# Performance work log

Measured on AMD Instinct MI355X. Metric: run time of the kernel, lower is better.

The kernel has to match this reference:

```python
import jax, jax.numpy as jnp
import numpy as np

NUM_CLASSES = 21
EPS = 1e-6


def setup_inputs() -> dict:
    key = jax.random.key(0)
    k1, k2, k3 = jax.random.split(key, 3)
    feats = jax.random.normal(k1, (8, 256, 64, 64), dtype=jnp.float32)
    preds = jax.random.normal(k2, (8, NUM_CLASSES, 256, 256), dtype=jnp.float32)
    # labels in [0, 22): includes nclass=21 which acts as an ignore label
    masks = jax.random.randint(k3, (8, 256, 256), 0, 22, dtype=jnp.int64)
    return {"feats": feats, "preds": preds, "masks": masks}


def reference(feats, preds, masks):
    B, C = feats.shape[0], feats.shape[1]
    H, W = masks.shape[-2:]
    K = NUM_CLASSES

    # argmax over class logits -> predicted label map [B, H, W]
    pred_lbl = jnp.argmax(preds, axis=1)

    # bilinear upsample (align_corners=False, matches half-pixel resize)
    feats_up = jax.image.resize(feats, (B, C, H, W), method="bilinear")

    cls = jnp.arange(K)
    # one-hot of gt mask and of predictions; labels >= K (incl. 255) fall in
    # the dropped last channel of one_hot_2d, i.e. match no class here.
    gt_oh = (masks[:, None, :, :] == cls[None, :, None, None])      # [B,K,H,W]
    pr_oh = (pred_lbl[:, None, :, :] == cls[None, :, None, None])   # [B,K,H,W]
    joint = (gt_oh & pr_oh).astype(feats_up.dtype)                  # [B,K,H,W]

    counts = joint.sum(axis=(2, 3))                                  # [B,K]
    sums = jnp.einsum("bchw,bkhw->bkc", feats_up, joint)            # [B,K,C]

    # per-image class means (absent classes -> 0/eps = 0), then batch mean
    proto = (sums / (counts[..., None] + EPS)).mean(axis=0)          # [K,C]
    return proto
```

## Files before the change

kernel.cpp:

```cpp
#include <hip/hip_runtime.h>

#define KC   21
#define BB   8
#define CC   256
#define HWP  65536
#define SRC  4096
#define NS   32
#define PC   128

#define WSF_COUNTS 131072
#define WSF_ACC2   131328
#define ZTOT_F4    ((256 + BB*KC*CC) / 4)

__global__ __launch_bounds__(256, 2)
void k1_classify(const float* __restrict__ preds,
                 const int*   __restrict__ masks,
                 unsigned char* __restrict__ L,
                 float* __restrict__ zbase)
{
    int tid = threadIdx.x;
    int idx = blockIdx.x * 256 + tid;

    if (idx < ZTOT_F4)
        reinterpret_cast<float4*>(zbase)[idx] = make_float4(0.f, 0.f, 0.f, 0.f);

    int b   = idx >> 14;
    int hw4 = (idx & 16383) << 2;

    const float* pb = preds + (size_t)b * KC * HWP + hw4;
    float va[4][KC];
#pragma unroll
    for (int k = 0; k < KC; ++k) {
        float4 t = *reinterpret_cast<const float4*>(pb + (size_t)k * HWP);
        va[0][k] = t.x; va[1][k] = t.y; va[2][k] = t.z; va[3][k] = t.w;
    }

    int4 mm = *reinterpret_cast<const int4*>(masks + b * HWP + hw4);
    int mk[4] = { mm.x, mm.y, mm.z, mm.w };

    uchar4 r;
    unsigned char* rp = reinterpret_cast<unsigned char*>(&r);
#pragma unroll
    for (int j = 0; j < 4; ++j) {
        float best = va[j][0];
        int   bi   = 0;
#pragma unroll
        for (int k = 1; k < KC; ++k) {
            if (va[j][k] > best) { best = va[j][k]; bi = k; }
        }
        rp[j] = (mk[j] == bi) ? (unsigned char)bi : (unsigned char)255;
    }
    *reinterpret_cast<uchar4*>(L + (size_t)b * HWP + hw4) = r;
}

__global__ __launch_bounds__(1024, 4)
void k2_contract(const float* __restrict__ feats,
                 const unsigned char* __restrict__ L,
                 float* __restrict__ acc2,
                 float* __restrict__ counts)
{
    __shared__ float ws[KC * PC];
    __shared__ float scr[3 * KC * CC];
    int s = blockIdx.x, b = blockIdx.y;
    int tid = threadIdx.x;
    int p0 = s * PC;
    int ybase = 2 * s;

    int cp   = tid & 255;
    int psub = tid >> 8;
    int pw   = psub * 32;

    for (int t = tid; t < KC * PC / 4; t += 1024)
        *reinterpret_cast<float4*>(ws + t * 4) = make_float4(0.f, 0.f, 0.f, 0.f);

    float f[32];
    {
        const float* frow = feats + (size_t)(b * CC + cp) * SRC + p0 + pw;
#pragma unroll
        for (int q = 0; q < 8; ++q) {
            float4 t = *reinterpret_cast<const float4*>(frow + q * 4);
            f[q * 4 + 0] = t.x; f[q * 4 + 1] = t.y;
            f[q * 4 + 2] = t.z; f[q * 4 + 3] = t.w;
        }
    }
    __syncthreads();

    {
        int r = tid >> 6, cb = tid & 63;
        int h = 8 * s - 2 + r;
        if (r < 12 && (unsigned)h < 256u) {
            float sy = h * 0.25f - 0.375f;
            int   yt = (int)floorf(sy);
            float wy = sy - (float)yt;
            int ya = yt < 0 ? 0 : yt;
            int yb = yt + 1 > 63 ? 63 : yt + 1;
            float wyy0 = ((ya == ybase)     ? (1.f - wy) : 0.f) + ((yb == ybase)     ? wy : 0.f);
            float wyy1 = ((ya == ybase + 1) ? (1.f - wy) : 0.f) + ((yb == ybase + 1) ? wy : 0.f);
            if (wyy0 != 0.f || wyy1 != 0.f) {
                const unsigned char* Lrow = L + ((size_t)b << 16) + ((size_t)h << 8);
#pragma unroll
                for (int j = 0; j < 4; ++j) {
                    int w = cb + j * 64;
                    int k = Lrow[w];
                    if (k < KC) {
                        float sx = w * 0.25f - 0.375f;
                        int   xt = (int)floorf(sx);
                        float wx = sx - (float)xt;
                        int xa = xt < 0 ? 0 : xt;
                        int xb = xt + 1 > 63 ? 63 : xt + 1;
                        float* wk = ws + k * PC;
                        if (wyy0 != 0.f) {
                            atomicAdd(wk + xa, wyy0 * (1.f - wx));
                            atomicAdd(wk + xb, wyy0 * wx);
                        }
                        if (wyy1 != 0.f) {
                            atomicAdd(wk + 64 + xa, wyy1 * (1.f - wx));
                            atomicAdd(wk + 64 + xb, wyy1 * wx);
                        }
                    }
                }
            }
        }
    }
    __syncthreads();

    if (tid < KC) {
        float swcnt = 0.f;
#pragma unroll
        for (int i = 0; i < PC; ++i)
            swcnt += ws[tid * PC + ((i + tid * 8) & (PC - 1))];
        if (swcnt != 0.f)
            atomicAdd(&counts[b * KC + tid], swcnt);
    }

    float acc[KC];
#pragma unroll
    for (int k = 0; k < KC; ++k) {
        const float* wk = ws + k * PC + pw;
        float a0 = 0.f, a1 = 0.f, a2 = 0.f, a3 = 0.f;
#pragma unroll
        for (int q = 0; q < 8; ++q) {
            float4 w4 = *reinterpret_cast<const float4*>(wk + q * 4);
            a0 += w4.x * f[q * 4 + 0];
            a1 += w4.y * f[q * 4 + 1];
            a2 += w4.z * f[q * 4 + 2];
            a3 += w4.w * f[q * 4 + 3];
        }
        acc[k] = (a0 + a1) + (a2 + a3);
    }

    if (psub >= 1) {
        float* sp = scr + (psub - 1) * (KC * CC);
#pragma unroll
        for (int k = 0; k < KC; ++k) sp[k * CC + cp] = acc[k];
    }
    __syncthreads();
    if (psub == 0) {
        float* ap = acc2 + (size_t)(b * KC) * CC + cp;
#pragma unroll
        for (int k = 0; k < KC; ++k) {
            float v = acc[k] + scr[k * CC + cp]
                             + scr[KC * CC + k * CC + cp]
                             + scr[2 * KC * CC + k * CC + cp];
            atomicAdd(ap + (size_t)k * CC, v);
        }
    }
}

__global__ __launch_bounds__(256)
void k3_finalize(const float* __restrict__ acc2,
                 const float* __restrict__ counts,
                 float* __restrict__ out)
{
    int k = blockIdx.x;
    int c = threadIdx.x;

    float r = 0.f;
#pragma unroll
    for (int b = 0; b < BB; ++b) {
        float cnt = counts[b * KC + k];
        r += acc2[(size_t)(b * KC + k) * CC + c] / (cnt + 1e-6f);
    }
    out[k * CC + c] = r * 0.125f;
}

extern "C" void kernel_launch(void* const* d_in, const int* in_sizes, int n_in,
                              void* d_out, int out_size, void* d_ws, size_t ws_size,
                              hipStream_t stream) {
    const float* feats = (const float*)d_in[0];
    const float* preds = (const float*)d_in[1];
    const int*   masks = (const int*)  d_in[2];
    float* out = (float*)d_out;

    float* wsf = (float*)d_ws;
    unsigned char* L = (unsigned char*)d_ws;
    float* counts = wsf + WSF_COUNTS;
    float* acc2   = wsf + WSF_ACC2;

    k1_classify<<<(BB * HWP / 4) / 256, 256, 0, stream>>>(preds, masks, L, counts);
    k2_contract<<<dim3(NS, BB), 1024, 0, stream>>>(feats, L, acc2, counts);
    k3_finalize<<<KC, 256, 0, stream>>>(acc2, counts, out);
}
```

Measured before the change: 33.78 us.

## Fuse argmax classification into contraction kernel and replace atomics with partial sums

Measured after the change: 45.33 us. 34.2% more time.

```diff
diff --git a/kernel.cpp b/kernel.cpp
--- a/kernel.cpp
+++ b/kernel.cpp
@@ -8,56 +8,14 @@
 #define NS   32
 #define PC   128
 
-#define WSF_COUNTS 131072
-#define WSF_ACC2   131328
-#define ZTOT_F4    ((256 + BB*KC*CC) / 4)
-
-__global__ __launch_bounds__(256, 2)
-void k1_classify(const float* __restrict__ preds,
-                 const int*   __restrict__ masks,
-                 unsigned char* __restrict__ L,
-                 float* __restrict__ zbase)
-{
-    int tid = threadIdx.x;
-    int idx = blockIdx.x * 256 + tid;
-
-    if (idx < ZTOT_F4)
-        reinterpret_cast<float4*>(zbase)[idx] = make_float4(0.f, 0.f, 0.f, 0.f);
-
-    int b   = idx >> 14;
-    int hw4 = (idx & 16383) << 2;
-
-    const float* pb = preds + (size_t)b * KC * HWP + hw4;
-    float va[4][KC];
-#pragma unroll
-    for (int k = 0; k < KC; ++k) {
-        float4 t = *reinterpret_cast<const float4*>(pb + (size_t)k * HWP);
-        va[0][k] = t.x; va[1][k] = t.y; va[2][k] = t.z; va[3][k] = t.w;
-    }
-
-    int4 mm = *reinterpret_cast<const int4*>(masks + b * HWP + hw4);
-    int mk[4] = { mm.x, mm.y, mm.z, mm.w };
-
-    uchar4 r;
-    unsigned char* rp = reinterpret_cast<unsigned char*>(&r);
-#pragma unroll
-    for (int j = 0; j < 4; ++j) {
-        float best = va[j][0];
-        int   bi   = 0;
-#pragma unroll
-        for (int k = 1; k < KC; ++k) {
-            if (va[j][k] > best) { best = va[j][k]; bi = k; }
-        }
-        rp[j] = (mk[j] == bi) ? (unsigned char)bi : (unsigned char)255;
-    }
-    *reinterpret_cast<uchar4*>(L + (size_t)b * HWP + hw4) = r;
-}
+#define WSF_PART 8192
 
 __global__ __launch_bounds__(1024, 4)
-void k2_contract(const float* __restrict__ feats,
-                 const unsigned char* __restrict__ L,
-                 float* __restrict__ acc2,
-                 float* __restrict__ counts)
+void kf_fused(const float* __restrict__ preds,
+              const int*   __restrict__ masks,
+              const float* __restrict__ feats,
+              float* __restrict__ partial,
+              float* __restrict__ partialw)
 {
     __shared__ float ws[KC * PC];
     __shared__ float scr[3 * KC * CC];
@@ -97,18 +55,30 @@
             float wyy0 = ((ya == ybase)     ? (1.f - wy) : 0.f) + ((yb == ybase)     ? wy : 0.f);
             float wyy1 = ((ya == ybase + 1) ? (1.f - wy) : 0.f) + ((yb == ybase + 1) ? wy : 0.f);
             if (wyy0 != 0.f || wyy1 != 0.f) {
-                const unsigned char* Lrow = L + ((size_t)b << 16) + ((size_t)h << 8);
-#pragma unroll
+                const float* prow = preds + (size_t)b * KC * HWP + ((size_t)h << 8);
+                const int*   mrow = masks + ((size_t)b << 16) + ((size_t)h << 8);
+#pragma unroll 1
                 for (int j = 0; j < 4; ++j) {
                     int w = cb + j * 64;
-                    int k = Lrow[w];
-                    if (k < KC) {
+                    float v[KC];
+#pragma unroll
+                    for (int k = 0; k < KC; ++k)
+                        v[k] = prow[(size_t)k * HWP + w];
+                    int m = mrow[w];
+
+                    float best = v[0];
+                    int   bi   = 0;
+#pragma unroll
+                    for (int k = 1; k < KC; ++k) {
+                        if (v[k] > best) { best = v[k]; bi = k; }
+                    }
+                    if (m == bi) {
                         float sx = w * 0.25f - 0.375f;
                         int   xt = (int)floorf(sx);
                         float wx = sx - (float)xt;
                         int xa = xt < 0 ? 0 : xt;
                         int xb = xt + 1 > 63 ? 63 : xt + 1;
-                        float* wk = ws + k * PC;
+                        float* wk = ws + bi * PC;
                         if (wyy0 != 0.f) {
                             atomicAdd(wk + xa, wyy0 * (1.f - wx));
                             atomicAdd(wk + xb, wyy0 * wx);
@@ -129,8 +99,7 @@
 #pragma unroll
         for (int i = 0; i < PC; ++i)
             swcnt += ws[tid * PC + ((i + tid * 8) & (PC - 1))];
-        if (swcnt != 0.f)
-            atomicAdd(&counts[b * KC + tid], swcnt);
+        partialw[(size_t)(b * NS + s) * KC + tid] = swcnt;
     }
 
     float acc[KC];
@@ -156,30 +125,39 @@
     }
     __syncthreads();
     if (psub == 0) {
-        float* ap = acc2 + (size_t)(b * KC) * CC + cp;
+        float* op = partial + ((size_t)(b * NS + s)) * KC * CC + cp;
 #pragma unroll
         for (int k = 0; k < KC; ++k) {
             float v = acc[k] + scr[k * CC + cp]
                              + scr[KC * CC + k * CC + cp]
                              + scr[2 * KC * CC + k * CC + cp];
-            atomicAdd(ap + (size_t)k * CC, v);
+            op[(size_t)k * CC] = v;
         }
     }
 }
 
 __global__ __launch_bounds__(256)
-void k3_finalize(const float* __restrict__ acc2,
-                 const float* __restrict__ counts,
+void k3_finalize(const float* __restrict__ partial,
+                 const float* __restrict__ partialw,
                  float* __restrict__ out)
 {
     int k = blockIdx.x;
     int c = threadIdx.x;
 
     float r = 0.f;
+#pragma unroll 1
+    for (int b = 0; b < BB; ++b) {
+        float cnt = 0.f;
 #pragma unroll
-    for (int b = 0; b < BB; ++b) {
-        float cnt = counts[b * KC + k];
-        r += acc2[(size_t)(b * KC + k) * CC + c] / (cnt + 1e-6f);
+        for (int s = 0; s < NS; ++s)
+            cnt += partialw[(size_t)(b * NS + s) * KC + k];
+
+        float acc = 0.f;
+        const float* base = partial + ((size_t)(b * NS) * KC + k) * CC + c;
+#pragma unroll 8
+        for (int s = 0; s < NS; ++s) acc += base[(size_t)s * KC * CC];
+
+        r += acc / (cnt + 1e-6f);
     }
     out[k * CC + c] = r * 0.125f;
 }
@@ -193,11 +171,9 @@
     float* out = (float*)d_out;
 
     float* wsf = (float*)d_ws;
-    unsigned char* L = (unsigned char*)d_ws;
-    float* counts = wsf + WSF_COUNTS;
-    float* acc2   = wsf + WSF_ACC2;
+    float* partialw = wsf;
+    float* partial  = wsf + WSF_PART;
 
-    k1_classify<<<(BB * HWP / 4) / 256, 256, 0, stream>>>(preds, masks, L, counts);
-    k2_contract<<<dim3(NS, BB), 1024, 0, stream>>>(feats, L, acc2, counts);
-    k3_finalize<<<KC, 256, 0, stream>>>(acc2, counts, out);
+    kf_fused<<<dim3(NS, BB), 1024, 0, stream>>>(preds, masks, feats, partial, partialw);
+    k3_finalize<<<KC, 256, 0, stream>>>(partial, partialw, out);
 }
```
